# Performance work log

Measured on AMD Instinct MI355X. Metric: run time of the kernel, lower is better.

Reference implementation:

```python
import jax, jax.numpy as jnp
import numpy as np

B, S, H, F, E, TOPK = 2, 2048, 1024, 4096, 8, 2


def setup_inputs() -> dict:
    key = jax.random.key(0)
    k0, k1, k2, k3, k4 = jax.random.split(key, 5)
    scale = 0.02
    return {
        "hidden_states": jax.random.normal(k0, (B, S, H), dtype=jnp.float32),
        "gate_w": jax.random.normal(k1, (E, H), dtype=jnp.float32) * scale,
        "w1": jax.random.normal(k2, (E, F, H), dtype=jnp.float32) * scale,
        "w2": jax.random.normal(k3, (E, H, F), dtype=jnp.float32) * scale,
        "w3": jax.random.normal(k4, (E, F, H), dtype=jnp.float32) * scale,
        "top_k": TOPK,
    }


def reference(hidden_states, gate_w, w1, w2, w3, top_k):
    b, s, h = hidden_states.shape
    num_experts = gate_w.shape[0]
    x = hidden_states.reshape(-1, h)                      # [T,H]
    router_logits = x @ gate_w.T                          # [T,E]
    routing = jax.nn.softmax(router_logits.astype(jnp.float32), axis=-1)
    top_w, top_e = jax.lax.top_k(routing, top_k)          # [T,K]
    top_w = top_w / top_w.sum(axis=-1, keepdims=True)     # renormalize over top-k
    top_w = top_w.astype(x.dtype)
    # combine weights [T,E]: zero for unselected experts (faithful to masked dispatch)
    cw = (jax.nn.one_hot(top_e, num_experts, dtype=x.dtype) * top_w[..., None]).sum(axis=1)
    out = jnp.zeros_like(x)
    for e in range(num_experts):  # fixed, small expert count
        inter = jax.nn.silu(x @ w1[e].T) * (x @ w3[e].T)  # [T,F]
        out = out + cw[:, e:e + 1] * (inter @ w2[e].T)
    return out.reshape(b, s, h), router_logits
```

## Files before the change

### kernel.cpp

```cpp
#include <hip/hip_runtime.h>
#include <stdint.h>

#define T 4096
#define HDIM 1024
#define FDIM 4096
#define NE 8
#define MAXROWS 9216

typedef __bf16 bf16x8 __attribute__((ext_vector_type(8)));
typedef float f32x4 __attribute__((ext_vector_type(4)));

__device__ __forceinline__ unsigned short f2bf(float f) {
    unsigned u = __builtin_bit_cast(unsigned, f);
    u += 0x7FFFu + ((u >> 16) & 1u);
    return (unsigned short)(u >> 16);
}

__device__ __forceinline__ void cp16(const void* g, const void* lds) {
    __builtin_amdgcn_global_load_lds(
        (const __attribute__((address_space(1))) unsigned int*)g,
        (__attribute__((address_space(3))) unsigned int*)(unsigned int)(unsigned long long)lds,
        16, 0, 0);
}

__global__ void conv_x_k(const float* __restrict__ x, unsigned short* __restrict__ xb) {
    size_t i = ((size_t)blockIdx.x * 256 + threadIdx.x) * 8;
    float4 a = *(const float4*)(x + i);
    float4 b = *(const float4*)(x + i + 4);
    uint4 v;
    v.x = (unsigned)f2bf(a.x) | ((unsigned)f2bf(a.y) << 16);
    v.y = (unsigned)f2bf(a.z) | ((unsigned)f2bf(a.w) << 16);
    v.z = (unsigned)f2bf(b.x) | ((unsigned)f2bf(b.y) << 16);
    v.w = (unsigned)f2bf(b.z) | ((unsigned)f2bf(b.w) << 16);
    *(uint4*)(xb + i) = v;
}

__global__ void conv_all_k(const float* __restrict__ w1, const float* __restrict__ w3,
                           const float* __restrict__ w2,
                           unsigned short* __restrict__ wb1, unsigned short* __restrict__ wb3,
                           unsigned short* __restrict__ wb2) {
    int z = blockIdx.y;
    const float* s = (z == 0) ? w1 : (z == 1) ? w3 : w2;
    unsigned short* d = (z == 0) ? wb1 : (z == 1) ? wb3 : wb2;
    size_t i = ((size_t)blockIdx.x * 256 + threadIdx.x) * 8;
    float4 a = *(const float4*)(s + i);
    float4 b = *(const float4*)(s + i + 4);
    uint4 v;
    v.x = (unsigned)f2bf(a.x) | ((unsigned)f2bf(a.y) << 16);
    v.y = (unsigned)f2bf(a.z) | ((unsigned)f2bf(a.w) << 16);
    v.z = (unsigned)f2bf(b.x) | ((unsigned)f2bf(b.y) << 16);
    v.w = (unsigned)f2bf(b.z) | ((unsigned)f2bf(b.w) << 16);
    *(uint4*)(d + i) = v;
}

__global__ void conv_w13_k(const float* __restrict__ src, unsigned short* __restrict__ dst,
                           int f0, int Fc) {
    int e = blockIdx.y;
    size_t rem = ((size_t)blockIdx.x * 256 + threadIdx.x) * 8;
    const float* s = src + ((size_t)e * FDIM + f0) * HDIM + rem;
    unsigned short* d = dst + (size_t)e * Fc * HDIM + rem;
    float4 a = *(const float4*)(s);
    float4 b = *(const float4*)(s + 4);
    uint4 v;
    v.x = (unsigned)f2bf(a.x) | ((unsigned)f2bf(a.y) << 16);
    v.y = (unsigned)f2bf(a.z) | ((unsigned)f2bf(a.w) << 16);
    v.z = (unsigned)f2bf(b.x) | ((unsigned)f2bf(b.y) << 16);
    v.w = (unsigned)f2bf(b.z) | ((unsigned)f2bf(b.w) << 16);
    *(uint4*)(d) = v;
}

__global__ void conv_w2_k(const float* __restrict__ src, unsigned short* __restrict__ dst,
                          int f0, int Fc, int fcShift) {
    int e = blockIdx.y;
    size_t idx = ((size_t)blockIdx.x * 256 + threadIdx.x) * 8;
    int h = (int)(idx >> fcShift);
    int c = (int)(idx & (size_t)(Fc - 1));
    const float* s = src + ((size_t)e * HDIM + h) * FDIM + f0 + c;
    unsigned short* d = dst + (size_t)e * HDIM * Fc + idx;
    float4 a = *(const float4*)(s);
    float4 b = *(const float4*)(s + 4);
    uint4 v;
    v.x = (unsigned)f2bf(a.x) | ((unsigned)f2bf(a.y) << 16);
    v.y = (unsigned)f2bf(a.z) | ((unsigned)f2bf(a.w) << 16);
    v.z = (unsigned)f2bf(b.x) | ((unsigned)f2bf(b.y) << 16);
    v.w = (unsigned)f2bf(b.z) | ((unsigned)f2bf(b.w) << 16);
    *(uint4*)(d) = v;
}

__global__ void router_k(const float* __restrict__ x, const float* __restrict__ gw,
                         float* __restrict__ logits_out, int* __restrict__ cnt,
                         int* __restrict__ list, float* __restrict__ wlist) {
    int w = threadIdx.x >> 6, lane = threadIdx.x & 63;
    int t = blockIdx.x * 4 + w;
    float acc[NE];
#pragma unroll
    for (int e = 0; e < NE; ++e) acc[e] = 0.f;
    for (int i = 0; i < HDIM / 64; ++i) {
        int h = i * 64 + lane;
        float xv = x[(size_t)t * HDIM + h];
#pragma unroll
        for (int e = 0; e < NE; ++e) acc[e] += xv * gw[e * HDIM + h];
    }
#pragma unroll
    for (int e = 0; e < NE; ++e)
#pragma unroll
        for (int off = 32; off; off >>= 1) acc[e] += __shfl_xor(acc[e], off);
    if (lane == 0) {
#pragma unroll
        for (int e = 0; e < NE; ++e) logits_out[(size_t)t * NE + e] = acc[e];
        int e1 = 0;
#pragma unroll
        for (int e = 1; e < NE; ++e) if (acc[e] > acc[e1]) e1 = e;
        int e2 = (e1 == 0) ? 1 : 0;
#pragma unroll
        for (int e = 0; e < NE; ++e) { if (e == e1) continue; if (acc[e] > acc[e2]) e2 = e; }
        float wa = 1.f / (1.f + expf(acc[e2] - acc[e1]));
        float wb = 1.f - wa;
        int p1 = atomicAdd(&cnt[e1], 1); list[e1 * T + p1] = t; wlist[e1 * T + p1] = wa;
        int p2 = atomicAdd(&cnt[e2], 1); list[e2 * T + p2] = t; wlist[e2 * T + p2] = wb;
    }
}

__global__ void offsets_k(const int* __restrict__ cnt, int* __restrict__ poff) {
    if (threadIdx.x == 0) {
        int o = 0; poff[0] = 0;
        for (int e = 0; e < NE; ++e) { o += ((cnt[e] + 127) >> 7) << 7; poff[e + 1] = o; }
    }
}

__global__ void compact_k(const int* __restrict__ cnt, const int* __restrict__ poff,
                          const int* __restrict__ list, const float* __restrict__ wlist,
                          int* __restrict__ tok_row, float* __restrict__ w_row) {
    int gid = blockIdx.x * 256 + threadIdx.x;
    int e = gid >> 12, i = gid & (T - 1);
    int pc = poff[e + 1] - poff[e];
    if (i < pc) {
        int row = poff[e] + i;
        if (i < cnt[e]) { tok_row[row] = list[e * T + i]; w_row[row] = wlist[e * T + i]; }
        else           { tok_row[row] = T;               w_row[row] = 0.f; }
    }
}

__global__ __launch_bounds__(256, 3) void gemm1_k(
    const unsigned short* __restrict__ xb, const unsigned short* __restrict__ wb1,
    const unsigned short* __restrict__ wb3, const int* __restrict__ tok_row,
    const int* __restrict__ poff, unsigned short* __restrict__ inter, int Fc) {

    __shared__ __align__(16) unsigned short As[128 * 64];
    __shared__ __align__(16) unsigned short B1[128 * 64];
    __shared__ __align__(16) unsigned short B3[128 * 64];
    __shared__ int toks[128];
    __shared__ int e_sh;

    int row0 = blockIdx.y * 128;
    if (row0 >= poff[NE]) return;
    int tid = threadIdx.x;
    if (tid == 0) { int e = 0; while (row0 >= poff[e + 1]) ++e; e_sh = e; }
    if (tid < 128) toks[tid] = tok_row[row0 + tid];
    __syncthreads();
    int e = e_sh;
    int fr0 = blockIdx.x * 128;
    const unsigned short* w1p = wb1 + ((size_t)e * Fc + fr0) * HDIM;
    const unsigned short* w3p = wb3 + ((size_t)e * Fc + fr0) * HDIM;

    int wv = tid >> 6, lane = tid & 63;
    int quad = lane >> 4, l16 = lane & 15;
    int wm = (wv >> 1) * 64, wn = (wv & 1) * 64;

    int sr = lane >> 3;
    int sc = (lane & 7) ^ sr;
    unsigned a_off[4];
#pragma unroll
    for (int jj = 0; jj < 4; ++jj)
        a_off[jj] = (unsigned)toks[wv * 32 + jj * 8 + sr] * HDIM + sc * 8;
    const unsigned short* w1b = w1p + (size_t)(wv * 32 + sr) * HDIM + sc * 8;
    const unsigned short* w3b = w3p + (size_t)(wv * 32 + sr) * HDIM + sc * 8;

    f32x4 acc1[4][4], acc3[4][4];
#pragma unroll
    for (int a = 0; a < 4; ++a)
#pragma unroll
        for (int b = 0; b < 4; ++b) {
            acc1[a][b] = f32x4{0.f, 0.f, 0.f, 0.f};
            acc3[a][b] = f32x4{0.f, 0.f, 0.f, 0.f};
        }

    for (int k0 = 0; k0 < HDIM; k0 += 64) {
#pragma unroll
        for (int jj = 0; jj < 4; ++jj) {
            int j = wv * 4 + jj;
            cp16(xb + a_off[jj] + k0, As + j * 512);
            cp16(w1b + (size_t)jj * 8 * HDIM + k0, B1 + j * 512);
            cp16(w3b + (size_t)jj * 8 * HDIM + k0, B3 + j * 512);
        }
        __syncthreads();
#pragma unroll
        for (int ks = 0; ks < 2; ++ks) {
            int cb0 = ks * 4 + quad;
            bf16x8 af[4];
#pragma unroll
            for (int mi = 0; mi < 4; ++mi) {
                int m = wm + mi * 16 + l16;
                af[mi] = *(const bf16x8*)(As + m * 64 + ((cb0 ^ (m & 7)) * 8));
            }
#pragma unroll
            for (int ni = 0; ni < 4; ++ni) {
                int n = wn + ni * 16 + l16;
                int boff = n * 64 + ((cb0 ^ (n & 7)) * 8);
                bf16x8 b1f = *(const bf16x8*)(B1 + boff);
                bf16x8 b3f = *(const bf16x8*)(B3 + boff);
#pragma unroll
                for (int mi = 0; mi < 4; ++mi) {
                    acc1[mi][ni] = __builtin_amdgcn_mfma_f32_16x16x32_bf16(af[mi], b1f, acc1[mi][ni], 0, 0, 0);
                    acc3[mi][ni] = __builtin_amdgcn_mfma_f32_16x16x32_bf16(af[mi], b3f, acc3[mi][ni], 0, 0, 0);
                }
            }
        }
        __syncthreads();
    }
#pragma unroll
    for (int mi = 0; mi < 4; ++mi)
#pragma unroll
        for (int ni = 0; ni < 4; ++ni)
#pragma unroll
            for (int r = 0; r < 4; ++r) {
                int m = wm + mi * 16 + quad * 4 + r;
                int n = wn + ni * 16 + l16;
                float v1 = acc1[mi][ni][r], v3 = acc3[mi][ni][r];
                float hval = (v1 / (1.f + __expf(-v1))) * v3;
                inter[(size_t)(row0 + m) * Fc + fr0 + n] = f2bf(hval);
            }
}

__global__ __launch_bounds__(256, 3) void gemm2_k(
    const unsigned short* __restrict__ inter, const unsigned short* __restrict__ wb2,
    const int* __restrict__ tok_row, const float* __restrict__ w_row,
    const int* __restrict__ poff, float* __restrict__ out, int Fc) {

    __shared__ __align__(16) unsigned short As[128 * 64];
    __shared__ __align__(16) unsigned short Bs[128 * 64];
    __shared__ int e_sh;

    int row0 = blockIdx.y * 128;
    if (row0 >= poff[NE]) return;
    int tid = threadIdx.x;
    if (tid == 0) { int e = 0; while (row0 >= poff[e + 1]) ++e; e_sh = e; }
    __syncthreads();
    int e = e_sh;
    int n0 = blockIdx.x * 128;

    int wv = tid >> 6, lane = tid & 63;
    int quad = lane >> 4, l16 = lane & 15;
    int wm = (wv >> 1) * 64, wn = (wv & 1) * 64;

    int sr = lane >> 3;
    int sc = (lane & 7) ^ sr;
    const unsigned short* a_b = inter + (size_t)(row0 + wv * 32 + sr) * Fc + sc * 8;
    const unsigned short* b_b = wb2 + ((size_t)e * HDIM + n0 + wv * 32 + sr) * Fc + sc * 8;

    f32x4 acc[4][4];
#pragma unroll
    for (int a = 0; a < 4; ++a)
#pragma unroll
        for (int b = 0; b < 4; ++b) acc[a][b] = f32x4{0.f, 0.f, 0.f, 0.f};

    for (int k0 = 0; k0 < Fc; k0 += 64) {
#pragma unroll
        for (int jj = 0; jj < 4; ++jj) {
            int j = wv * 4 + jj;
            cp16(a_b + (size_t)jj * 8 * Fc + k0, As + j * 512);
            cp16(b_b + (size_t)jj * 8 * Fc + k0, Bs + j * 512);
        }
        __syncthreads();
#pragma unroll
        for (int ks = 0; ks < 2; ++ks) {
            int cb0 = ks * 4 + quad;
            bf16x8 af[4];
#pragma unroll
            for (int mi = 0; mi < 4; ++mi) {
                int m = wm + mi * 16 + l16;
                af[mi] = *(const bf16x8*)(As + m * 64 + ((cb0 ^ (m & 7)) * 8));
            }
#pragma unroll
            for (int ni = 0; ni < 4; ++ni) {
                int n = wn + ni * 16 + l16;
                bf16x8 bf = *(const bf16x8*)(Bs + n * 64 + ((cb0 ^ (n & 7)) * 8));
#pragma unroll
                for (int mi = 0; mi < 4; ++mi)
                    acc[mi][ni] = __builtin_amdgcn_mfma_f32_16x16x32_bf16(af[mi], bf, acc[mi][ni], 0, 0, 0);
            }
        }
        __syncthreads();
    }
#pragma unroll
    for (int mi = 0; mi < 4; ++mi)
#pragma unroll
        for (int r = 0; r < 4; ++r) {
            int m = wm + mi * 16 + quad * 4 + r;
            int grow = row0 + m;
            float wr = w_row[grow];
            if (wr != 0.f) {
                int t = tok_row[grow];
                float* op = out + (size_t)t * HDIM + n0;
#pragma unroll
                for (int ni = 0; ni < 4; ++ni)
                    atomicAdd(op + wn + ni * 16 + l16, wr * acc[mi][ni][r]);
            }
        }
}

extern "C" void kernel_launch(void* const* d_in, const int* in_sizes, int n_in,
                              void* d_out, int out_size, void* d_ws, size_t ws_size,
                              hipStream_t stream) {
    const float* x  = (const float*)d_in[0];
    const float* gw = (const float*)d_in[1];
    const float* w1 = (const float*)d_in[2];
    const float* w2 = (const float*)d_in[3];
    const float* w3 = (const float*)d_in[4];
    float* out = (float*)d_out;
    float* logits = out + (size_t)T * HDIM;

    char* ws = (char*)d_ws;
    size_t off = 0;
    auto alloc = [&](size_t b) {
        off = (off + 255) & ~(size_t)255;
        void* p = ws + off;
        off += b;
        return p;
    };
    int* cnt        = (int*)alloc(NE * 4);
    int* poff       = (int*)alloc((NE + 1) * 4);
    int* list       = (int*)alloc((size_t)NE * T * 4);
    float* wlist    = (float*)alloc((size_t)NE * T * 4);
    int* tok_row    = (int*)alloc(MAXROWS * 4);
    float* w_row    = (float*)alloc(MAXROWS * 4);
    unsigned short* xb = (unsigned short*)alloc((size_t)(T + 1) * HDIM * 2);
    size_t fixed_off = off;

    int Fc = 4096, fcShift = 12;
    for (;;) {
        size_t need = fixed_off + 3 * ((size_t)NE * Fc * HDIM * 2) + (size_t)MAXROWS * Fc * 2 + 1024;
        if (need <= ws_size || Fc == 512) break;
        Fc >>= 1; fcShift -= 1;
    }
    unsigned short* wb1 = (unsigned short*)alloc((size_t)NE * Fc * HDIM * 2);
    unsigned short* wb3 = (unsigned short*)alloc((size_t)NE * Fc * HDIM * 2);
    unsigned short* wb2 = (unsigned short*)alloc((size_t)NE * HDIM * Fc * 2);
    unsigned short* inter = (unsigned short*)alloc((size_t)MAXROWS * Fc * 2);

    hipMemsetAsync(cnt, 0, NE * 4, stream);
    hipMemsetAsync(out, 0, (size_t)T * HDIM * 4, stream);
    hipMemsetAsync(xb + (size_t)T * HDIM, 0, HDIM * 2, stream);
    conv_x_k<<<(T * HDIM / 8) / 256, 256, 0, stream>>>(x, xb);
    router_k<<<T / 4, 256, 0, stream>>>(x, gw, logits, cnt, list, wlist);
    offsets_k<<<1, 64, 0, stream>>>(cnt, poff);
    compact_k<<<NE * T / 256, 256, 0, stream>>>(cnt, poff, list, wlist, tok_row, w_row);

    int nMT = MAXROWS / 128;
    if (Fc == FDIM) {
        conv_all_k<<<dim3((size_t)NE * FDIM * HDIM / 8 / 256, 3), 256, 0, stream>>>(
            w1, w3, w2, wb1, wb3, wb2);
        gemm1_k<<<dim3(FDIM / 128, nMT), 256, 0, stream>>>(xb, wb1, wb3, tok_row, poff, inter, FDIM);
        gemm2_k<<<dim3(HDIM / 128, nMT), 256, 0, stream>>>(inter, wb2, tok_row, w_row, poff, out, FDIM);
    } else {
        for (int f0 = 0; f0 < FDIM; f0 += Fc) {
            conv_w13_k<<<dim3(Fc / 2, NE), 256, 0, stream>>>(w1, wb1, f0, Fc);
            conv_w13_k<<<dim3(Fc / 2, NE), 256, 0, stream>>>(w3, wb3, f0, Fc);
            conv_w2_k<<<dim3(HDIM * Fc / 2048, NE), 256, 0, stream>>>(w2, wb2, f0, Fc, fcShift);
            gemm1_k<<<dim3(Fc / 128, nMT), 256, 0, stream>>>(xb, wb1, wb3, tok_row, poff, inter, Fc);
            gemm2_k<<<dim3(HDIM / 128, nMT), 256, 0, stream>>>(inter, wb2, tok_row, w_row, poff, out, Fc);
        }
    }
}
```

Before: 798.4 us.

## Rewrite expert up-projection GEMM as 256x128 tile with 4-stage LDS pipeline

```diff
diff --git a/kernel.cpp b/kernel.cpp
--- a/kernel.cpp
+++ b/kernel.cpp
@@ -5,7 +5,7 @@
 #define HDIM 1024
 #define FDIM 4096
 #define NE 8
-#define MAXROWS 9216
+#define MAXROWS 10240
 
 typedef __bf16 bf16x8 __attribute__((ext_vector_type(8)));
 typedef float f32x4 __attribute__((ext_vector_type(4)));
@@ -124,7 +124,7 @@
 __global__ void offsets_k(const int* __restrict__ cnt, int* __restrict__ poff) {
     if (threadIdx.x == 0) {
         int o = 0; poff[0] = 0;
-        for (int e = 0; e < NE; ++e) { o += ((cnt[e] + 127) >> 7) << 7; poff[e + 1] = o; }
+        for (int e = 0; e < NE; ++e) { o += ((cnt[e] + 255) >> 8) << 8; poff[e + 1] = o; }
     }
 }
 
@@ -141,40 +141,50 @@
     }
 }
 
-__global__ __launch_bounds__(256, 3) void gemm1_k(
+__global__ __launch_bounds__(512, 2) void gemm1_k(
     const unsigned short* __restrict__ xb, const unsigned short* __restrict__ wb1,
     const unsigned short* __restrict__ wb3, const int* __restrict__ tok_row,
     const int* __restrict__ poff, unsigned short* __restrict__ inter, int Fc) {
 
-    __shared__ __align__(16) unsigned short As[128 * 64];
-    __shared__ __align__(16) unsigned short B1[128 * 64];
-    __shared__ __align__(16) unsigned short B3[128 * 64];
-    __shared__ int toks[128];
+    __shared__ __align__(16) unsigned short lds[4 * 16384];
+    __shared__ int toks[256];
     __shared__ int e_sh;
 
-    int row0 = blockIdx.y * 128;
+    int row0 = blockIdx.y * 256;
     if (row0 >= poff[NE]) return;
     int tid = threadIdx.x;
     if (tid == 0) { int e = 0; while (row0 >= poff[e + 1]) ++e; e_sh = e; }
-    if (tid < 128) toks[tid] = tok_row[row0 + tid];
+    if (tid < 256) toks[tid] = tok_row[row0 + tid];
     __syncthreads();
     int e = e_sh;
     int fr0 = blockIdx.x * 128;
     const unsigned short* w1p = wb1 + ((size_t)e * Fc + fr0) * HDIM;
     const unsigned short* w3p = wb3 + ((size_t)e * Fc + fr0) * HDIM;
 
+    int rs = tid >> 2, cs = tid & 3;
+    int csw = (cs ^ (rs & 3)) * 8;
+    const unsigned short* a_src0 = xb + (size_t)toks[rs] * HDIM + csw;
+    const unsigned short* a_src1 = xb + (size_t)toks[128 + rs] * HDIM + csw;
+    const unsigned short* b1_src = w1p + (size_t)rs * HDIM + csw;
+    const unsigned short* b3_src = w3p + (size_t)rs * HDIM + csw;
+    char* ldsB = (char*)lds;
+    unsigned dA0 = tid * 16u, dA1 = 8192u + tid * 16u;
+    unsigned dB1 = 16384u + tid * 16u, dB3 = 24576u + tid * 16u;
+
     int wv = tid >> 6, lane = tid & 63;
     int quad = lane >> 4, l16 = lane & 15;
-    int wm = (wv >> 1) * 64, wn = (wv & 1) * 64;
-
-    int sr = lane >> 3;
-    int sc = (lane & 7) ^ sr;
-    unsigned a_off[4];
-#pragma unroll
-    for (int jj = 0; jj < 4; ++jj)
-        a_off[jj] = (unsigned)toks[wv * 32 + jj * 8 + sr] * HDIM + sc * 8;
-    const unsigned short* w1b = w1p + (size_t)(wv * 32 + sr) * HDIM + sc * 8;
-    const unsigned short* w3b = w3p + (size_t)(wv * 32 + sr) * HDIM + sc * 8;
+    int wm = (wv >> 1) * 64;
+    int wn = (wv & 1) * 64;
+    int cx = (quad ^ (l16 & 3)) * 16;
+    unsigned aoff[4], b1off[4], b3off[4];
+#pragma unroll
+    for (int mi = 0; mi < 4; ++mi) aoff[mi] = (unsigned)((wm + mi * 16 + l16) * 64 + cx);
+#pragma unroll
+    for (int ni = 0; ni < 4; ++ni) {
+        int n = wn + ni * 16 + l16;
+        b1off[ni] = (unsigned)(16384 + n * 64 + cx);
+        b3off[ni] = (unsigned)(24576 + n * 64 + cx);
+    }
 
     f32x4 acc1[4][4], acc3[4][4];
 #pragma unroll
@@ -185,39 +195,64 @@
             acc3[a][b] = f32x4{0.f, 0.f, 0.f, 0.f};
         }
 
-    for (int k0 = 0; k0 < HDIM; k0 += 64) {
-#pragma unroll
-        for (int jj = 0; jj < 4; ++jj) {
-            int j = wv * 4 + jj;
-            cp16(xb + a_off[jj] + k0, As + j * 512);
-            cp16(w1b + (size_t)jj * 8 * HDIM + k0, B1 + j * 512);
-            cp16(w3b + (size_t)jj * 8 * HDIM + k0, B3 + j * 512);
-        }
-        __syncthreads();
-#pragma unroll
-        for (int ks = 0; ks < 2; ++ks) {
-            int cb0 = ks * 4 + quad;
-            bf16x8 af[4];
-#pragma unroll
-            for (int mi = 0; mi < 4; ++mi) {
-                int m = wm + mi * 16 + l16;
-                af[mi] = *(const bf16x8*)(As + m * 64 + ((cb0 ^ (m & 7)) * 8));
-            }
-#pragma unroll
-            for (int ni = 0; ni < 4; ++ni) {
-                int n = wn + ni * 16 + l16;
-                int boff = n * 64 + ((cb0 ^ (n & 7)) * 8);
-                bf16x8 b1f = *(const bf16x8*)(B1 + boff);
-                bf16x8 b3f = *(const bf16x8*)(B3 + boff);
-#pragma unroll
-                for (int mi = 0; mi < 4; ++mi) {
-                    acc1[mi][ni] = __builtin_amdgcn_mfma_f32_16x16x32_bf16(af[mi], b1f, acc1[mi][ni], 0, 0, 0);
-                    acc3[mi][ni] = __builtin_amdgcn_mfma_f32_16x16x32_bf16(af[mi], b3f, acc3[mi][ni], 0, 0, 0);
-                }
-            }
-        }
-        __syncthreads();
-    }
+#pragma unroll
+    for (int s = 0; s < 3; ++s) {
+        char* db = ldsB + s * 32768;
+        cp16(a_src0 + s * 32, db + dA0);
+        cp16(a_src1 + s * 32, db + dA1);
+        cp16(b1_src + s * 32, db + dB1);
+        cp16(b3_src + s * 32, db + dB3);
+    }
+    asm volatile("s_waitcnt vmcnt(8)" ::: "memory");
+    __builtin_amdgcn_s_barrier();
+
+#pragma unroll 1
+    for (int s = 0; s < 32; ++s) {
+        const char* sb = ldsB + (s & 3) * 32768;
+        int sf = s + 3; if (sf > 31) sf = 31;
+        char* db = ldsB + ((s + 3) & 3) * 32768;
+
+        bf16x8 af[4], bf[4];
+#pragma unroll
+        for (int mi = 0; mi < 4; ++mi) af[mi] = *(const bf16x8*)(sb + aoff[mi]);
+#pragma unroll
+        for (int ni = 0; ni < 4; ++ni) bf[ni] = *(const bf16x8*)(sb + b1off[ni]);
+        cp16(a_src0 + sf * 32, db + dA0);
+        cp16(a_src1 + sf * 32, db + dA1);
+        __builtin_amdgcn_sched_barrier(0);
+        __builtin_amdgcn_s_barrier();
+        asm volatile("s_waitcnt lgkmcnt(0)" ::: "memory");
+        __builtin_amdgcn_sched_barrier(0);
+        __builtin_amdgcn_s_setprio(1);
+#pragma unroll
+        for (int ni = 0; ni < 4; ++ni)
+#pragma unroll
+            for (int mi = 0; mi < 4; ++mi)
+                acc1[mi][ni] = __builtin_amdgcn_mfma_f32_16x16x32_bf16(af[mi], bf[ni], acc1[mi][ni], 0, 0, 0);
+        __builtin_amdgcn_s_setprio(0);
+        __builtin_amdgcn_sched_barrier(0);
+        __builtin_amdgcn_s_barrier();
+
+#pragma unroll
+        for (int ni = 0; ni < 4; ++ni) bf[ni] = *(const bf16x8*)(sb + b3off[ni]);
+        cp16(b1_src + sf * 32, db + dB1);
+        cp16(b3_src + sf * 32, db + dB3);
+        asm volatile("s_waitcnt vmcnt(8)" ::: "memory");
+        __builtin_amdgcn_sched_barrier(0);
+        __builtin_amdgcn_s_barrier();
+        asm volatile("s_waitcnt lgkmcnt(0)" ::: "memory");
+        __builtin_amdgcn_sched_barrier(0);
+        __builtin_amdgcn_s_setprio(1);
+#pragma unroll
+        for (int ni = 0; ni < 4; ++ni)
+#pragma unroll
+            for (int mi = 0; mi < 4; ++mi)
+                acc3[mi][ni] = __builtin_amdgcn_mfma_f32_16x16x32_bf16(af[mi], bf[ni], acc3[mi][ni], 0, 0, 0);
+        __builtin_amdgcn_s_setprio(0);
+        __builtin_amdgcn_sched_barrier(0);
+        __builtin_amdgcn_s_barrier();
+    }
+
 #pragma unroll
     for (int mi = 0; mi < 4; ++mi)
 #pragma unroll
@@ -356,19 +391,20 @@
     offsets_k<<<1, 64, 0, stream>>>(cnt, poff);
     compact_k<<<NE * T / 256, 256, 0, stream>>>(cnt, poff, list, wlist, tok_row, w_row);
 
-    int nMT = MAXROWS / 128;
+    int nMT1 = MAXROWS / 256;
+    int nMT2 = MAXROWS / 128;
     if (Fc == FDIM) {
         conv_all_k<<<dim3((size_t)NE * FDIM * HDIM / 8 / 256, 3), 256, 0, stream>>>(
             w1, w3, w2, wb1, wb3, wb2);
-        gemm1_k<<<dim3(FDIM / 128, nMT), 256, 0, stream>>>(xb, wb1, wb3, tok_row, poff, inter, FDIM);
-        gemm2_k<<<dim3(HDIM / 128, nMT), 256, 0, stream>>>(inter, wb2, tok_row, w_row, poff, out, FDIM);
+        gemm1_k<<<dim3(FDIM / 128, nMT1), 512, 0, stream>>>(xb, wb1, wb3, tok_row, poff, inter, FDIM);
+        gemm2_k<<<dim3(HDIM / 128, nMT2), 256, 0, stream>>>(inter, wb2, tok_row, w_row, poff, out, FDIM);
     } else {
         for (int f0 = 0; f0 < FDIM; f0 += Fc) {
             conv_w13_k<<<dim3(Fc / 2, NE), 256, 0, stream>>>(w1, wb1, f0, Fc);
             conv_w13_k<<<dim3(Fc / 2, NE), 256, 0, stream>>>(w3, wb3, f0, Fc);
             conv_w2_k<<<dim3(HDIM * Fc / 2048, NE), 256, 0, stream>>>(w2, wb2, f0, Fc, fcShift);
-            gemm1_k<<<dim3(Fc / 128, nMT), 256, 0, stream>>>(xb, wb1, wb3, tok_row, poff, inter, Fc);
-            gemm2_k<<<dim3(HDIM / 128, nMT), 256, 0, stream>>>(inter, wb2, tok_row, w_row, poff, out, Fc);
+            gemm1_k<<<dim3(Fc / 128, nMT1), 512, 0, stream>>>(xb, wb1, wb3, tok_row, poff, inter, Fc);
+            gemm2_k<<<dim3(HDIM / 128, nMT2), 256, 0, stream>>>(inter, wb2, tok_row, w_row, poff, out, Fc);
         }
     }
 }
```

Measured after the change: 815.4 us. +2.1%, slower.

## Double-buffer gemm1 LDS with 256-row tiles and 512-thread blocks

Applied to the files above, without the earlier changes.

```diff
diff --git a/kernel.cpp b/kernel.cpp
--- a/kernel.cpp
+++ b/kernel.cpp
@@ -5,7 +5,7 @@
 #define HDIM 1024
 #define FDIM 4096
 #define NE 8
-#define MAXROWS 9216
+#define MAXROWS 10240
 
 typedef __bf16 bf16x8 __attribute__((ext_vector_type(8)));
 typedef float f32x4 __attribute__((ext_vector_type(4)));
@@ -124,7 +124,7 @@
 __global__ void offsets_k(const int* __restrict__ cnt, int* __restrict__ poff) {
     if (threadIdx.x == 0) {
         int o = 0; poff[0] = 0;
-        for (int e = 0; e < NE; ++e) { o += ((cnt[e] + 127) >> 7) << 7; poff[e + 1] = o; }
+        for (int e = 0; e < NE; ++e) { o += ((cnt[e] + 255) >> 8) << 8; poff[e + 1] = o; }
     }
 }
 
@@ -141,22 +141,20 @@
     }
 }
 
-__global__ __launch_bounds__(256, 3) void gemm1_k(
+__global__ __launch_bounds__(512, 2) void gemm1_k(
     const unsigned short* __restrict__ xb, const unsigned short* __restrict__ wb1,
     const unsigned short* __restrict__ wb3, const int* __restrict__ tok_row,
     const int* __restrict__ poff, unsigned short* __restrict__ inter, int Fc) {
 
-    __shared__ __align__(16) unsigned short As[128 * 64];
-    __shared__ __align__(16) unsigned short B1[128 * 64];
-    __shared__ __align__(16) unsigned short B3[128 * 64];
-    __shared__ int toks[128];
+    __shared__ __align__(16) unsigned short lds[2 * 32768];
+    __shared__ int toks[256];
     __shared__ int e_sh;
 
-    int row0 = blockIdx.y * 128;
+    int row0 = blockIdx.y * 256;
     if (row0 >= poff[NE]) return;
     int tid = threadIdx.x;
     if (tid == 0) { int e = 0; while (row0 >= poff[e + 1]) ++e; e_sh = e; }
-    if (tid < 128) toks[tid] = tok_row[row0 + tid];
+    if (tid < 256) toks[tid] = tok_row[row0 + tid];
     __syncthreads();
     int e = e_sh;
     int fr0 = blockIdx.x * 128;
@@ -165,16 +163,22 @@
 
     int wv = tid >> 6, lane = tid & 63;
     int quad = lane >> 4, l16 = lane & 15;
-    int wm = (wv >> 1) * 64, wn = (wv & 1) * 64;
+    int wm = (wv >> 1) * 64;
+    int wn = (wv & 1) * 64;
 
     int sr = lane >> 3;
     int sc = (lane & 7) ^ sr;
     unsigned a_off[4];
 #pragma unroll
     for (int jj = 0; jj < 4; ++jj)
-        a_off[jj] = (unsigned)toks[wv * 32 + jj * 8 + sr] * HDIM + sc * 8;
-    const unsigned short* w1b = w1p + (size_t)(wv * 32 + sr) * HDIM + sc * 8;
-    const unsigned short* w3b = w3p + (size_t)(wv * 32 + sr) * HDIM + sc * 8;
+        a_off[jj] = (unsigned)toks[(wv * 4 + jj) * 8 + sr] * HDIM + sc * 8;
+    const unsigned short* b1b = w1p + (size_t)(wv * 16 + sr) * HDIM + sc * 8;
+    const unsigned short* b3b = w3p + (size_t)(wv * 16 + sr) * HDIM + sc * 8;
+
+    char* ldsc = (char*)lds;
+    unsigned dstA  = (unsigned)(wv * 4) * 1024u;
+    unsigned dstB1 = 32768u + (unsigned)(wv * 2) * 1024u;
+    unsigned dstB3 = 49152u + (unsigned)(wv * 2) * 1024u;
 
     f32x4 acc1[4][4], acc3[4][4];
 #pragma unroll
@@ -185,39 +189,62 @@
             acc3[a][b] = f32x4{0.f, 0.f, 0.f, 0.f};
         }
 
-    for (int k0 = 0; k0 < HDIM; k0 += 64) {
-#pragma unroll
-        for (int jj = 0; jj < 4; ++jj) {
-            int j = wv * 4 + jj;
-            cp16(xb + a_off[jj] + k0, As + j * 512);
-            cp16(w1b + (size_t)jj * 8 * HDIM + k0, B1 + j * 512);
-            cp16(w3b + (size_t)jj * 8 * HDIM + k0, B3 + j * 512);
-        }
-        __syncthreads();
+#pragma unroll
+    for (int jj = 0; jj < 4; ++jj)
+        cp16(xb + a_off[jj], ldsc + dstA + jj * 1024);
+#pragma unroll
+    for (int jj = 0; jj < 2; ++jj) {
+        cp16(b1b + (size_t)jj * 8 * HDIM, ldsc + dstB1 + jj * 1024);
+        cp16(b3b + (size_t)jj * 8 * HDIM, ldsc + dstB3 + jj * 1024);
+    }
+    __syncthreads();
+
+#pragma unroll 1
+    for (int k = 0; k < 16; ++k) {
+        const unsigned short* sb = lds + (k & 1) * 32768;
+
+        if (k < 15) {
+            char* db = ldsc + ((k + 1) & 1) * 65536;
+            int ko = (k + 1) * 64;
+#pragma unroll
+            for (int jj = 0; jj < 4; ++jj)
+                cp16(xb + a_off[jj] + ko, db + dstA + jj * 1024);
+#pragma unroll
+            for (int jj = 0; jj < 2; ++jj) {
+                cp16(b1b + (size_t)jj * 8 * HDIM + ko, db + dstB1 + jj * 1024);
+                cp16(b3b + (size_t)jj * 8 * HDIM + ko, db + dstB3 + jj * 1024);
+            }
+        }
+
 #pragma unroll
         for (int ks = 0; ks < 2; ++ks) {
             int cb0 = ks * 4 + quad;
-            bf16x8 af[4];
+            bf16x8 af[4], b1f[4], b3f[4];
 #pragma unroll
             for (int mi = 0; mi < 4; ++mi) {
                 int m = wm + mi * 16 + l16;
-                af[mi] = *(const bf16x8*)(As + m * 64 + ((cb0 ^ (m & 7)) * 8));
+                af[mi] = *(const bf16x8*)(sb + m * 64 + ((cb0 ^ (m & 7)) * 8));
             }
 #pragma unroll
             for (int ni = 0; ni < 4; ++ni) {
                 int n = wn + ni * 16 + l16;
-                int boff = n * 64 + ((cb0 ^ (n & 7)) * 8);
-                bf16x8 b1f = *(const bf16x8*)(B1 + boff);
-                bf16x8 b3f = *(const bf16x8*)(B3 + boff);
+                int sw = (cb0 ^ (n & 7)) * 8;
+                b1f[ni] = *(const bf16x8*)(sb + 16384 + n * 64 + sw);
+                b3f[ni] = *(const bf16x8*)(sb + 24576 + n * 64 + sw);
+            }
+            __builtin_amdgcn_s_setprio(1);
+#pragma unroll
+            for (int ni = 0; ni < 4; ++ni)
 #pragma unroll
                 for (int mi = 0; mi < 4; ++mi) {
-                    acc1[mi][ni] = __builtin_amdgcn_mfma_f32_16x16x32_bf16(af[mi], b1f, acc1[mi][ni], 0, 0, 0);
-                    acc3[mi][ni] = __builtin_amdgcn_mfma_f32_16x16x32_bf16(af[mi], b3f, acc3[mi][ni], 0, 0, 0);
+                    acc1[mi][ni] = __builtin_amdgcn_mfma_f32_16x16x32_bf16(af[mi], b1f[ni], acc1[mi][ni], 0, 0, 0);
+                    acc3[mi][ni] = __builtin_amdgcn_mfma_f32_16x16x32_bf16(af[mi], b3f[ni], acc3[mi][ni], 0, 0, 0);
                 }
-            }
+            __builtin_amdgcn_s_setprio(0);
         }
         __syncthreads();
     }
+
 #pragma unroll
     for (int mi = 0; mi < 4; ++mi)
 #pragma unroll
@@ -356,19 +383,20 @@
     offsets_k<<<1, 64, 0, stream>>>(cnt, poff);
     compact_k<<<NE * T / 256, 256, 0, stream>>>(cnt, poff, list, wlist, tok_row, w_row);
 
-    int nMT = MAXROWS / 128;
+    int nMT1 = MAXROWS / 256;
+    int nMT2 = MAXROWS / 128;
     if (Fc == FDIM) {
         conv_all_k<<<dim3((size_t)NE * FDIM * HDIM / 8 / 256, 3), 256, 0, stream>>>(
             w1, w3, w2, wb1, wb3, wb2);
-        gemm1_k<<<dim3(FDIM / 128, nMT), 256, 0, stream>>>(xb, wb1, wb3, tok_row, poff, inter, FDIM);
-        gemm2_k<<<dim3(HDIM / 128, nMT), 256, 0, stream>>>(inter, wb2, tok_row, w_row, poff, out, FDIM);
+        gemm1_k<<<dim3(FDIM / 128, nMT1), 512, 0, stream>>>(xb, wb1, wb3, tok_row, poff, inter, FDIM);
+        gemm2_k<<<dim3(HDIM / 128, nMT2), 256, 0, stream>>>(inter, wb2, tok_row, w_row, poff, out, FDIM);
     } else {
         for (int f0 = 0; f0 < FDIM; f0 += Fc) {
             conv_w13_k<<<dim3(Fc / 2, NE), 256, 0, stream>>>(w1, wb1, f0, Fc);
             conv_w13_k<<<dim3(Fc / 2, NE), 256, 0, stream>>>(w3, wb3, f0, Fc);
             conv_w2_k<<<dim3(HDIM * Fc / 2048, NE), 256, 0, stream>>>(w2, wb2, f0, Fc, fcShift);
-            gemm1_k<<<dim3(Fc / 128, nMT), 256, 0, stream>>>(xb, wb1, wb3, tok_row, poff, inter, Fc);
-            gemm2_k<<<dim3(HDIM / 128, nMT), 256, 0, stream>>>(inter, wb2, tok_row, w_row, poff, out, Fc);
-        }
-    }
-}
+            gemm1_k<<<dim3(Fc / 128, nMT1), 512, 0, stream>>>(xb, wb1, wb3, tok_row, poff, inter, Fc);
+            gemm2_k<<<dim3(HDIM / 128, nMT2), 256, 0, stream>>>(inter, wb2, tok_row, w_row, poff, out, Fc);
+        }
+    }
+}
```

Result: no change. 790.7 us (-1.0%).
